# Optimization experiments

Measured on AMD Instinct MI355X. Metric: run time of the kernel, lower is better.

Reference implementation:

```python
import jax, jax.numpy as jnp
import numpy as np
import math

B, T, C = 2, 2048, 2048
H, KV, HD = 16, 4, 128          # n_head, n_kv_head, head_dim
REP = H // KV
FFN = 5632                      # multiple_of-rounded 2/3 * 4 * n_embd
EPS = 1e-5


def setup_inputs() -> dict:
    key = jax.random.key(0)
    ks = jax.random.split(key, 10)
    s = 0.02
    x = jax.random.normal(ks[0], (B, T, C), dtype=jnp.float32)
    # RoPE table: (T, HD/2, 2) = (cos, sin)
    inv_freq = 1.0 / (10000.0 ** (np.arange(0, HD, 2, dtype=np.float32) / HD))
    ang = np.arange(T, dtype=np.float32)[:, None] * inv_freq[None, :]
    freqs_cis = jnp.asarray(np.stack([np.cos(ang), np.sin(ang)], axis=-1))
    wq = s * jax.random.normal(ks[1], (H * HD, C), dtype=jnp.float32)
    wk = s * jax.random.normal(ks[2], (KV * HD, C), dtype=jnp.float32)
    wv = s * jax.random.normal(ks[3], (KV * HD, C), dtype=jnp.float32)
    wo = s * jax.random.normal(ks[4], (C, H * HD), dtype=jnp.float32)
    w1 = s * jax.random.normal(ks[5], (FFN, C), dtype=jnp.float32)
    w2 = s * jax.random.normal(ks[6], (FFN, C), dtype=jnp.float32)
    c_proj = s * jax.random.normal(ks[7], (C, FFN), dtype=jnp.float32)
    g1 = jnp.ones((C,), dtype=jnp.float32)
    g2 = jnp.ones((C,), dtype=jnp.float32)
    return {"x": x, "freqs_cis": freqs_cis, "wq": wq, "wk": wk, "wv": wv,
            "wo": wo, "w1": w1, "w2": w2, "c_proj": c_proj, "g1": g1, "g2": g2}


def _rmsnorm(x, g, eps=EPS):
    return x * jax.lax.rsqrt(jnp.mean(x * x, axis=-1, keepdims=True) + eps) * g


def _rope(t, freqs_cis):
    # t: (B, T, nH, HD); freqs_cis: (T, HD/2, 2)
    tr = t.reshape(*t.shape[:-1], HD // 2, 2)
    cos = freqs_cis[None, :, None, :, 0]
    sin = freqs_cis[None, :, None, :, 1]
    out = jnp.stack([tr[..., 0] * cos - tr[..., 1] * sin,
                     tr[..., 0] * sin + tr[..., 1] * cos], axis=-1)
    return out.reshape(t.shape)


def reference(x, freqs_cis, wq, wk, wv, wo, w1, w2, c_proj, g1, g2):
    h = _rmsnorm(x, g1)
    q = (h @ wq.T).reshape(B, T, H, HD)
    k = (h @ wk.T).reshape(B, T, KV, HD)
    v = (h @ wv.T).reshape(B, T, KV, HD)
    q = _rope(q, freqs_cis)
    k = _rope(k, freqs_cis)
    # GQA: group query heads by kv head; never materialize expanded K/V
    q = q.transpose(0, 2, 1, 3).reshape(B, KV, REP, T, HD)  # b g r q d
    k = k.transpose(0, 2, 1, 3)                              # b g k d
    v = v.transpose(0, 2, 1, 3)                              # b g k d
    scale = 1.0 / math.sqrt(HD)
    scores = jnp.einsum('bgrqd,bgkd->bgrqk', q, k) * scale
    causal = jnp.tril(jnp.ones((T, T), dtype=bool))
    scores = jnp.where(causal, scores, jnp.float32(-1e30))
    attn = jax.nn.softmax(scores, axis=-1)
    y = jnp.einsum('bgrqk,bgkd->bgrqd', attn, v)
    y = y.reshape(B, H, T, HD).transpose(0, 2, 1, 3).reshape(B, T, C)
    x = x + y @ wo.T
    h2 = _rmsnorm(x, g2)
    mlp = (jax.nn.silu(h2 @ w1.T) * (h2 @ w2.T)) @ c_proj.T
    return x + mlp
```

## Files before the change

### kernel.cpp

```cpp
#include <hip/hip_runtime.h>
#include <hip/hip_bf16.h>
#include <math.h>

#define TT   2048
#define CC   2048
#define NB   2
#define NH   16
#define NKV  4
#define HDIM 128
#define NFFN 5632

typedef __attribute__((ext_vector_type(8))) short     bf8;
typedef __attribute__((ext_vector_type(4))) float     f32x4;
typedef __attribute__((ext_vector_type(8))) unsigned short u16x8;
typedef __attribute__((ext_vector_type(4))) unsigned short u16x4;

__device__ __forceinline__ float b2f(unsigned short u) {
    union { unsigned u; float f; } v; v.u = ((unsigned)u) << 16; return v.f;
}
__device__ __forceinline__ unsigned short f2bf(float f) {
    union { float f; unsigned u; } v; v.f = f;
    unsigned r = (v.u + 0x7fffu + ((v.u >> 16) & 1u)) >> 16;
    return (unsigned short)r;
}
__device__ __forceinline__ void gll16(const void* g, void* l) {
    __builtin_amdgcn_global_load_lds((const __attribute__((address_space(1))) void*)g,
                                     (__attribute__((address_space(3))) void*)l, 16, 0, 0);
}

__global__ __launch_bounds__(256) void cvt_k(const float* __restrict__ in,
        __hip_bfloat16* __restrict__ out)
{
    const size_t i = ((size_t)blockIdx.x * 256 + threadIdx.x) * 8;
    float4 a = *(const float4*)(in + i);
    float4 b = *(const float4*)(in + i + 4);
    u16x8 v;
    v[0] = f2bf(a.x); v[1] = f2bf(a.y); v[2] = f2bf(a.z); v[3] = f2bf(a.w);
    v[4] = f2bf(b.x); v[5] = f2bf(b.y); v[6] = f2bf(b.z); v[7] = f2bf(b.w);
    *(u16x8*)((unsigned short*)out + i) = v;
}

__global__ __launch_bounds__(256) void cvt3_k(const float* __restrict__ wq,
        const float* __restrict__ wk, const float* __restrict__ wv,
        __hip_bfloat16* __restrict__ out)
{
    const int row = blockIdx.x;
    const float* src = (row < 2048) ? (wq + (size_t)row * CC)
                     : (row < 2560) ? (wk + (size_t)(row - 2048) * CC)
                                    : (wv + (size_t)(row - 2560) * CC);
    const int e0 = threadIdx.x * 8;
    float4 a = *(const float4*)(src + e0);
    float4 b = *(const float4*)(src + e0 + 4);
    u16x8 v;
    v[0] = f2bf(a.x); v[1] = f2bf(a.y); v[2] = f2bf(a.z); v[3] = f2bf(a.w);
    v[4] = f2bf(b.x); v[5] = f2bf(b.y); v[6] = f2bf(b.z); v[7] = f2bf(b.w);
    *(u16x8*)((unsigned short*)out + (size_t)row * CC + e0) = v;
}

__global__ __launch_bounds__(256) void rms_f32_k(const float* __restrict__ x,
        const float* __restrict__ g, __hip_bfloat16* __restrict__ o)
{
    const size_t row = blockIdx.x;
    const int e0 = threadIdx.x * 8;
    float4 a = *(const float4*)(x + row * CC + e0);
    float4 b = *(const float4*)(x + row * CC + e0 + 4);
    float vals[8] = {a.x, a.y, a.z, a.w, b.x, b.y, b.z, b.w};
    float s = 0.f;
    #pragma unroll
    for (int e = 0; e < 8; ++e) s += vals[e] * vals[e];
    #pragma unroll
    for (int off = 32; off; off >>= 1) s += __shfl_xor(s, off);
    __shared__ float wsum[4];
    if ((threadIdx.x & 63) == 0) wsum[threadIdx.x >> 6] = s;
    __syncthreads();
    float scale = rsqrtf((wsum[0] + wsum[1] + wsum[2] + wsum[3]) * (1.0f / CC) + 1e-5f);
    float4 g0 = *(const float4*)(g + e0);
    float4 g1 = *(const float4*)(g + e0 + 4);
    float gs[8] = {g0.x, g0.y, g0.z, g0.w, g1.x, g1.y, g1.z, g1.w};
    u16x8 ov;
    #pragma unroll
    for (int e = 0; e < 8; ++e) ov[e] = f2bf(vals[e] * scale * gs[e]);
    *(u16x8*)((unsigned short*)o + row * CC + e0) = ov;
}

__global__ __launch_bounds__(256) void rms_bf16_k(const __hip_bfloat16* __restrict__ x,
        const float* __restrict__ g, __hip_bfloat16* __restrict__ o)
{
    const size_t row = blockIdx.x;
    const int e0 = threadIdx.x * 8;
    u16x8 xv = *(const u16x8*)((const unsigned short*)x + row * CC + e0);
    float vals[8];
    #pragma unroll
    for (int e = 0; e < 8; ++e) vals[e] = b2f(xv[e]);
    float s = 0.f;
    #pragma unroll
    for (int e = 0; e < 8; ++e) s += vals[e] * vals[e];
    #pragma unroll
    for (int off = 32; off; off >>= 1) s += __shfl_xor(s, off);
    __shared__ float wsum[4];
    if ((threadIdx.x & 63) == 0) wsum[threadIdx.x >> 6] = s;
    __syncthreads();
    float scale = rsqrtf((wsum[0] + wsum[1] + wsum[2] + wsum[3]) * (1.0f / CC) + 1e-5f);
    float4 g0 = *(const float4*)(g + e0);
    float4 g1 = *(const float4*)(g + e0 + 4);
    float gs[8] = {g0.x, g0.y, g0.z, g0.w, g1.x, g1.y, g1.z, g1.w};
    u16x8 ov;
    #pragma unroll
    for (int e = 0; e < 8; ++e) ov[e] = f2bf(vals[e] * scale * gs[e]);
    *(u16x8*)((unsigned short*)o + row * CC + e0) = ov;
}

#define GBM 128
#define GBN 128
#define GBK 32

template<int EPI, int OUTB>
__global__ __launch_bounds__(256) void gemm_db(
        const __hip_bfloat16* __restrict__ A,
        const __hip_bfloat16* __restrict__ W,
        const void* __restrict__ Rp,
        void* __restrict__ Cp,
        int M, int N, int K)
{
    __shared__ alignas(16) __hip_bfloat16 As[2][GBM][GBK];
    __shared__ alignas(16) __hip_bfloat16 Ws[2][GBN][GBK];
    const int tid  = threadIdx.x;
    const int lane = tid & 63;
    const int wid  = tid >> 6;
    const int wr = wid >> 1, wc = wid & 1;
    const int nwg = gridDim.x * gridDim.y;
    const int lin = blockIdx.y * gridDim.x + blockIdx.x;
    const int nlin = (lin & 7) * (nwg >> 3) + (lin >> 3);
    const int bxs = nlin % gridDim.x, bys = nlin / gridDim.x;
    const int bm = bys * GBM, bn = bxs * GBN;
    const int l4  = lane >> 2;
    const int lk8 = (lane & 3) * 8;
    const int fr  = lane & 15;
    const int fk  = (lane >> 4) * 8;

    f32x4 acc[4][4];
    #pragma unroll
    for (int m = 0; m < 4; ++m)
        #pragma unroll
        for (int n = 0; n < 4; ++n) acc[m][n] = (f32x4){0.f, 0.f, 0.f, 0.f};

    const __hip_bfloat16* ga0 = A + (size_t)(bm + wid * 32 + l4) * K + lk8;
    const __hip_bfloat16* ga1 = A + (size_t)(bm + wid * 32 + 16 + l4) * K + lk8;
    const __hip_bfloat16* gw0 = W + (size_t)(bn + wid * 32 + l4) * K + lk8;
    const __hip_bfloat16* gw1 = W + (size_t)(bn + wid * 32 + 16 + l4) * K + lk8;

    const int nt = K >> 5;
    gll16(ga0, &As[0][wid * 32][0]);
    gll16(ga1, &As[0][wid * 32 + 16][0]);
    gll16(gw0, &Ws[0][wid * 32][0]);
    gll16(gw1, &Ws[0][wid * 32 + 16][0]);

    #pragma unroll 2
    for (int t = 0; t < nt; ++t) {
        const int cur = t & 1;
        __syncthreads();
        if (t + 1 < nt) {
            const int k1 = (t + 1) << 5;
            const int nx = cur ^ 1;
            gll16(ga0 + k1, &As[nx][wid * 32][0]);
            gll16(ga1 + k1, &As[nx][wid * 32 + 16][0]);
            gll16(gw0 + k1, &Ws[nx][wid * 32][0]);
            gll16(gw1 + k1, &Ws[nx][wid * 32 + 16][0]);
        }
        bf8 af[4];
        #pragma unroll
        for (int m = 0; m < 4; ++m)
            af[m] = *(const bf8*)&As[cur][wr * 64 + m * 16 + fr][fk];
        #pragma unroll
        for (int n = 0; n < 4; ++n) {
            bf8 wf = *(const bf8*)&Ws[cur][wc * 64 + n * 16 + fr][fk];
            #pragma unroll
            for (int m = 0; m < 4; ++m)
                acc[m][n] = __builtin_amdgcn_mfma_f32_16x16x32_bf16(af[m], wf, acc[m][n], 0, 0, 0);
        }
    }

    const int rj = (lane >> 4) * 4;
    #pragma unroll
    for (int m = 0; m < 4; ++m) {
        #pragma unroll
        for (int j = 0; j < 4; ++j) {
            const size_t row = (size_t)(bm + wr * 64 + m * 16 + rj + j);
            #pragma unroll
            for (int n = 0; n < 4; ++n) {
                const size_t col = (size_t)(bn + wc * 64 + n * 16 + fr);
                float v = acc[m][n][j];
                if (EPI == 1) v += ((const float*)Rp)[row * N + col];
                if (EPI == 2) v += b2f(((const unsigned short*)Rp)[row * N + col]);
                if (EPI == 3) {
                    float gv = b2f(((const unsigned short*)Rp)[row * N + col]);
                    v = (gv / (1.0f + __expf(-gv))) * v;
                }
                if (OUTB) ((unsigned short*)Cp)[row * N + col] = f2bf(v);
                else      ((float*)Cp)[row * N + col] = v;
            }
        }
    }
}

__global__ __launch_bounds__(256) void gemm_qkv_db(
        const __hip_bfloat16* __restrict__ A,
        const __hip_bfloat16* __restrict__ W,
        const float* __restrict__ fc,
        __hip_bfloat16* __restrict__ qo,
        __hip_bfloat16* __restrict__ ko,
        __hip_bfloat16* __restrict__ vto,
        int M, int K)
{
    __shared__ alignas(16) __hip_bfloat16 As[2][GBM][GBK];
    __shared__ alignas(16) __hip_bfloat16 Ws[2][GBN][GBK];
    const int tid  = threadIdx.x;
    const int lane = tid & 63;
    const int wid  = tid >> 6;
    const int wr = wid >> 1, wc = wid & 1;
    const int nwg = gridDim.x * gridDim.y;
    const int lin = blockIdx.y * gridDim.x + blockIdx.x;
    const int nlin = (lin & 7) * (nwg >> 3) + (lin >> 3);
    const int bxs = nlin % gridDim.x, bys = nlin / gridDim.x;
    const int bm = bys * GBM, bn = bxs * GBN;
    const int l4  = lane >> 2;
    const int lk8 = (lane & 3) * 8;
    const int fr  = lane & 15;
    const int fk  = (lane >> 4) * 8;

    f32x4 acc[4][4];
    #pragma unroll
    for (int m = 0; m < 4; ++m)
        #pragma unroll
        for (int n = 0; n < 4; ++n) acc[m][n] = (f32x4){0.f, 0.f, 0.f, 0.f};

    const __hip_bfloat16* ga0 = A + (size_t)(bm + wid * 32 + l4) * K + lk8;
    const __hip_bfloat16* ga1 = A + (size_t)(bm + wid * 32 + 16 + l4) * K + lk8;
    const __hip_bfloat16* gw0 = W + (size_t)(bn + wid * 32 + l4) * K + lk8;
    const __hip_bfloat16* gw1 = W + (size_t)(bn + wid * 32 + 16 + l4) * K + lk8;

    const int nt = K >> 5;
    gll16(ga0, &As[0][wid * 32][0]);
    gll16(ga1, &As[0][wid * 32 + 16][0]);
    gll16(gw0, &Ws[0][wid * 32][0]);
    gll16(gw1, &Ws[0][wid * 32 + 16][0]);

    #pragma unroll 2
    for (int t = 0; t < nt; ++t) {
        const int cur = t & 1;
        __syncthreads();
        if (t + 1 < nt) {
            const int k1 = (t + 1) << 5;
            const int nx = cur ^ 1;
            gll16(ga0 + k1, &As[nx][wid * 32][0]);
            gll16(ga1 + k1, &As[nx][wid * 32 + 16][0]);
            gll16(gw0 + k1, &Ws[nx][wid * 32][0]);
            gll16(gw1 + k1, &Ws[nx][wid * 32 + 16][0]);
        }
        bf8 af[4];
        #pragma unroll
        for (int m = 0; m < 4; ++m)
            af[m] = *(const bf8*)&As[cur][wr * 64 + m * 16 + fr][fk];
        #pragma unroll
        for (int n = 0; n < 4; ++n) {
            bf8 wf = *(const bf8*)&Ws[cur][wc * 64 + n * 16 + fr][fk];
            #pragma unroll
            for (int m = 0; m < 4; ++m)
                acc[m][n] = __builtin_amdgcn_mfma_f32_16x16x32_bf16(af[m], wf, acc[m][n], 0, 0, 0);
        }
    }

    const int rj = (lane >> 4) * 4;
    #pragma unroll
    for (int m = 0; m < 4; ++m) {
        #pragma unroll
        for (int n = 0; n < 4; ++n) {
            const int col = bn + wc * 64 + n * 16 + fr;
            const int row0 = bm + wr * 64 + m * 16 + rj;
            if (col < 2560) {
                const int i2 = ((col & 127) >> 1) * 2;
                const int role = col & 1;
                #pragma unroll
                for (int j = 0; j < 4; ++j) {
                    const int t0 = (row0 + j) & (TT - 1);
                    const float cv = fc[t0 * HDIM + i2];
                    const float sv = fc[t0 * HDIM + i2 + 1];
                    const float v = acc[m][n][j];
                    const float partner = __shfl_xor(v, 1);
                    const float o = role ? (partner * sv + v * cv) : (v * cv - partner * sv);
                    if (col < 2048)
                        ((unsigned short*)qo)[(size_t)(row0 + j) * CC + col] = f2bf(o);
                    else
                        ((unsigned short*)ko)[(size_t)(row0 + j) * (NKV * HDIM) + (col - 2048)] = f2bf(o);
                }
            } else {
                const int vc = col - 2560;
                const int g = vc >> 7, d = vc & 127;
                const int b = row0 >> 11, t0 = row0 & (TT - 1);
                unsigned short* vp = (unsigned short*)vto +
                    ((size_t)(b * NKV + g) * HDIM + d) * TT + t0;
                u16x4 ov;
                #pragma unroll
                for (int j = 0; j < 4; ++j) ov[j] = f2bf(acc[m][n][j]);
                *(u16x4*)vp = ov;
            }
        }
    }
}

#define PBM 128
#define PBN 256
#define PBK 64

template<int EPI, int OUTB>
__global__ __launch_bounds__(512) void gemm_8p(
        const __hip_bfloat16* __restrict__ A,
        const __hip_bfloat16* __restrict__ W,
        const void* __restrict__ Rp,
        void* __restrict__ Cp,
        int M, int N, int K)
{
    __shared__ alignas(16) __hip_bfloat16 As[2][PBM][PBK];
    __shared__ alignas(16) __hip_bfloat16 Ws[2][PBN][PBK];
    const int tid  = threadIdx.x;
    const int lane = tid & 63;
    const int wid  = tid >> 6;
    const int wr = wid >> 2, wc = wid & 3;
    const int nwg = gridDim.x * gridDim.y;
    const int lin = blockIdx.y * gridDim.x + blockIdx.x;
    const int nlin = (lin & 7) * (nwg >> 3) + (lin >> 3);
    const int bxs = nlin % gridDim.x, bys = nlin / gridDim.x;
    const int bm = bys * PBM, bn = bxs * PBN;
    const int fr = lane & 15;
    const int hi = lane >> 4;

    f32x4 acc[4][4];
    #pragma unroll
    for (int m = 0; m < 4; ++m)
        #pragma unroll
        for (int n = 0; n < 4; ++n) acc[m][n] = (f32x4){0.f, 0.f, 0.f, 0.f};

    const unsigned short* Ag = (const unsigned short*)A;
    const unsigned short* Wg = (const unsigned short*)W;

    auto STAGE = [&](int buf, int k0) {
        #pragma unroll
        for (int l = 0; l < 2; ++l) {
            const int s = l * 512 + tid;
            const int row = s >> 3;
            const int srcb = ((s & 7) * 16) ^ ((row & 7) << 4);
            gll16(Ag + (size_t)(bm + row) * K + k0 + (srcb >> 1),
                  (unsigned short*)&As[buf][0][0] + (l * 512 + wid * 64) * 8);
        }
        #pragma unroll
        for (int l = 0; l < 4; ++l) {
            const int s = l * 512 + tid;
            const int row = s >> 3;
            const int srcb = ((s & 7) * 16) ^ ((row & 7) << 4);
            gll16(Wg + (size_t)(bn + row) * K + k0 + (srcb >> 1),
                  (unsigned short*)&Ws[buf][0][0] + (l * 512 + wid * 64) * 8);
        }
    };

    const int nt = K >> 6;
    STAGE(0, 0);
    __syncthreads();

    for (int t = 0; t < nt; ++t) {
        const int cur = t & 1;
        const char* Ab = (const char*)&As[cur][0][0];
        const char* Bb = (const char*)&Ws[cur][0][0];

        bf8 bF[4][2];
        #pragma unroll
        for (int n = 0; n < 4; ++n) {
            const int row = wc * 64 + n * 16 + fr;
            #pragma unroll
            for (int kk = 0; kk < 2; ++kk) {
                const int off = (kk * 64 + hi * 16) ^ ((row & 7) << 4);
                bF[n][kk] = *(const bf8*)(Bb + row * 128 + off);
            }
        }
        bf8 a0, a1;
        {
            const int row = wr * 64 + fr;
            a0 = *(const bf8*)(Ab + row * 128 + ((hi * 16)      ^ ((row & 7) << 4)));
            a1 = *(const bf8*)(Ab + row * 128 + ((64 + hi * 16) ^ ((row & 7) << 4)));
        }
        if (t + 1 < nt) STAGE(cur ^ 1, (t + 1) * PBK);
        __builtin_amdgcn_s_barrier();
        __builtin_amdgcn_s_setprio(1);
        #pragma unroll
        for (int n = 0; n < 4; ++n) {
            acc[0][n] = __builtin_amdgcn_mfma_f32_16x16x32_bf16(a0, bF[n][0], acc[0][n], 0, 0, 0);
            acc[0][n] = __builtin_amdgcn_mfma_f32_16x16x32_bf16(a1, bF[n][1], acc[0][n], 0, 0, 0);
        }
        __builtin_amdgcn_s_setprio(0);
        __builtin_amdgcn_s_barrier();

        #pragma unroll
        for (int m = 1; m < 4; ++m) {
            const int row = wr * 64 + m * 16 + fr;
            bf8 am0 = *(const bf8*)(Ab + row * 128 + ((hi * 16)      ^ ((row & 7) << 4)));
            bf8 am1 = *(const bf8*)(Ab + row * 128 + ((64 + hi * 16) ^ ((row & 7) << 4)));
            __builtin_amdgcn_s_barrier();
            __builtin_amdgcn_s_setprio(1);
            #pragma unroll
            for (int n = 0; n < 4; ++n) {
                acc[m][n] = __builtin_amdgcn_mfma_f32_16x16x32_bf16(am0, bF[n][0], acc[m][n], 0, 0, 0);
                acc[m][n] = __builtin_amdgcn_mfma_f32_16x16x32_bf16(am1, bF[n][1], acc[m][n], 0, 0, 0);
            }
            __builtin_amdgcn_s_setprio(0);
            if (m < 3) __builtin_amdgcn_s_barrier();
        }
        __syncthreads();
    }

    const int rj = hi * 4;
    #pragma unroll
    for (int m = 0; m < 4; ++m) {
        #pragma unroll
        for (int j = 0; j < 4; ++j) {
            const size_t row = (size_t)(bm + wr * 64 + m * 16 + rj + j);
            #pragma unroll
            for (int n = 0; n < 4; ++n) {
                const size_t col = (size_t)(bn + wc * 64 + n * 16 + fr);
                float v = acc[m][n][j];
                if (EPI == 1) v += ((const float*)Rp)[row * N + col];
                if (EPI == 2) v += b2f(((const unsigned short*)Rp)[row * N + col]);
                if (EPI == 3) {
                    float gv = b2f(((const unsigned short*)Rp)[row * N + col]);
                    v = (gv / (1.0f + __expf(-gv))) * v;
                }
                if (OUTB) ((unsigned short*)Cp)[row * N + col] = f2bf(v);
                else      ((float*)Cp)[row * N + col] = v;
            }
        }
    }
}

#define AQB 128
#define AKV 64

__global__ __launch_bounds__(512) void attn_mfma(const __hip_bfloat16* __restrict__ q,
        const __hip_bfloat16* __restrict__ k, const __hip_bfloat16* __restrict__ vt,
        __hip_bfloat16* __restrict__ y)
{
    __shared__ alignas(16) unsigned short Ks[AKV * HDIM];
    __shared__ alignas(16) unsigned short Vs[HDIM * AKV];
    __shared__ alignas(16) unsigned short Ps[AQB * AKV];

    const int qt = (TT / AQB - 1) - blockIdx.x;
    const int h  = blockIdx.y;
    const int b  = blockIdx.z;
    const int g  = h >> 2;
    const int qbase = qt * AQB;

    const int tid  = threadIdx.x;
    const int lane = tid & 63;
    const int wid  = tid >> 6;
    const int fr   = lane & 15;
    const int fk8  = (lane >> 4) * 8;
    const int rj   = (lane >> 4) * 4;

    bf8 qf[4];
    {
        const unsigned short* qp = (const unsigned short*)q +
            (size_t)(b * TT + qbase + wid * 16 + fr) * CC + h * HDIM;
        #pragma unroll
        for (int c = 0; c < 4; ++c)
            qf[c] = *(const bf8*)(qp + c * 32 + fk8);
    }
    const unsigned short* vtb = (const unsigned short*)vt + (size_t)(b * NKV + g) * HDIM * TT;

    f32x4 oacc[8];
    float m_r[4], l_r[4];
    #pragma unroll
    for (int n = 0; n < 8; ++n) oacc[n] = (f32x4){0.f, 0.f, 0.f, 0.f};
    #pragma unroll
    for (int j = 0; j < 4; ++j) { m_r[j] = -1e30f; l_r[j] = 0.f; }

    const float scale = 0.08838834764831845f;
    const int ntiles = qbase / AKV + 2;
    const int kjr = tid >> 3;
    const int kkc = (tid & 7) * 16;
    const int vdr = tid >> 2;
    const int vjc = (tid & 3) * 16;

    u16x8 krg[2], vrg[2];
    auto LOADT = [&](int jb) {
        const unsigned short* kp = (const unsigned short*)k +
            ((size_t)(b * TT + jb + kjr) * (NKV * HDIM)) + g * HDIM + kkc;
        const unsigned short* vp = vtb + (size_t)vdr * TT + jb + vjc;
        #pragma unroll
        for (int c = 0; c < 2; ++c) {
            krg[c] = *(const u16x8*)(kp + c * 8);
            vrg[c] = *(const u16x8*)(vp + c * 8);
        }
    };
    auto WRITET = [&]() {
        #pragma unroll
        for (int c = 0; c < 2; ++c) {
            const int byteK = (kjr * 256 + (kkc + c * 8) * 2) ^ ((kjr & 7) << 4);
            *(u16x8*)((char*)Ks + byteK) = krg[c];
            const int byteV = (vdr * 128 + (vjc + c * 8) * 2) ^ ((vdr & 7) << 4);
            *(u16x8*)((char*)Vs + byteV) = vrg[c];
        }
    };

    LOADT(0);

    for (int tile = 0; tile < ntiles; ++tile) {
        __syncthreads();
        WRITET();
        if (tile + 1 < ntiles) LOADT((tile + 1) * AKV);
        __syncthreads();

        f32x4 s[4];
        #pragma unroll
        for (int n = 0; n < 4; ++n) s[n] = (f32x4){0.f, 0.f, 0.f, 0.f};
        __builtin_amdgcn_s_setprio(1);
        #pragma unroll
        for (int c = 0; c < 4; ++c) {
            #pragma unroll
            for (int n = 0; n < 4; ++n) {
                const int j = n * 16 + fr;
                const int byteB = (j * 256 + (c * 32 + fk8) * 2) ^ ((j & 7) << 4);
                bf8 kf = *(const bf8*)((char*)Ks + byteB);
                s[n] = __builtin_amdgcn_mfma_f32_16x16x32_bf16(qf[c], kf, s[n], 0, 0, 0);
            }
        }
        __builtin_amdgcn_s_setprio(0);

        const int jbase = tile * AKV;
        #pragma unroll
        for (int jj = 0; jj < 4; ++jj) {
            const int qg = qbase + wid * 16 + rj + jj;
            float sv[4];
            #pragma unroll
            for (int n = 0; n < 4; ++n) {
                const int jg = jbase + n * 16 + fr;
                sv[n] = (jg <= qg) ? s[n][jj] * scale : -1e30f;
            }
            float tmax = fmaxf(fmaxf(sv[0], sv[1]), fmaxf(sv[2], sv[3]));
            tmax = fmaxf(tmax, __shfl_xor(tmax, 1));
            tmax = fmaxf(tmax, __shfl_xor(tmax, 2));
            tmax = fmaxf(tmax, __shfl_xor(tmax, 4));
            tmax = fmaxf(tmax, __shfl_xor(tmax, 8));
            if (tmax > m_r[jj] + 8.0f) {
                const float alpha = __expf(m_r[jj] - tmax);
                m_r[jj] = tmax;
                l_r[jj] *= alpha;
                #pragma unroll
                for (int n = 0; n < 8; ++n) oacc[n][jj] *= alpha;
            }
            const float mnew = m_r[jj];
            const int prow = wid * 16 + rj + jj;
            float tsum = 0.f;
            #pragma unroll
            for (int n = 0; n < 4; ++n) {
                const float p = __expf(sv[n] - mnew);
                tsum += p;
                const int byteP = (prow * 128 + (n * 16 + fr) * 2) ^ ((prow & 7) << 4);
                *(unsigned short*)((char*)Ps + byteP) = f2bf(p);
            }
            tsum += __shfl_xor(tsum, 1);
            tsum += __shfl_xor(tsum, 2);
            tsum += __shfl_xor(tsum, 4);
            tsum += __shfl_xor(tsum, 8);
            l_r[jj] += tsum;
        }

        __builtin_amdgcn_s_setprio(1);
        #pragma unroll
        for (int c2 = 0; c2 < 2; ++c2) {
            const int prow = wid * 16 + fr;
            const int byteA = (prow * 128 + (c2 * 32 + fk8) * 2) ^ ((prow & 7) << 4);
            bf8 pf = *(const bf8*)((char*)Ps + byteA);
            #pragma unroll
            for (int n = 0; n < 8; ++n) {
                const int d = n * 16 + fr;
                const int byteB = (d * 128 + (c2 * 32 + fk8) * 2) ^ ((d & 7) << 4);
                bf8 vf = *(const bf8*)((char*)Vs + byteB);
                oacc[n] = __builtin_amdgcn_mfma_f32_16x16x32_bf16(pf, vf, oacc[n], 0, 0, 0);
            }
        }
        __builtin_amdgcn_s_setprio(0);
    }

    #pragma unroll
    for (int jj = 0; jj < 4; ++jj) {
        const float inv = 1.0f / l_r[jj];
        unsigned short* yrow = (unsigned short*)y +
            ((size_t)(b * TT + qbase + wid * 16 + rj + jj) * CC) + h * HDIM;
        #pragma unroll
        for (int n = 0; n < 8; ++n)
            yrow[n * 16 + fr] = f2bf(oacc[n][jj] * inv);
    }
}

extern "C" void kernel_launch(void* const* d_in, const int* in_sizes, int n_in,
                              void* d_out, int out_size, void* d_ws, size_t ws_size,
                              hipStream_t stream)
{
    (void)in_sizes; (void)n_in; (void)out_size; (void)ws_size;
    const float* x     = (const float*)d_in[0];
    const float* fc    = (const float*)d_in[1];
    const float* wq    = (const float*)d_in[2];
    const float* wk    = (const float*)d_in[3];
    const float* wv    = (const float*)d_in[4];
    const float* wo    = (const float*)d_in[5];
    const float* w1    = (const float*)d_in[6];
    const float* w2    = (const float*)d_in[7];
    const float* cproj = (const float*)d_in[8];
    const float* g1    = (const float*)d_in[9];
    const float* g2    = (const float*)d_in[10];
    float* out = (float*)d_out;

    const int ROWS = NB * TT;
    unsigned char* wsb = (unsigned char*)d_ws;
    __hip_bfloat16* x2b = (__hip_bfloat16*)(wsb);
    __hip_bfloat16* hb  = (__hip_bfloat16*)(wsb + 16777216u);
    __hip_bfloat16* w1b = (__hip_bfloat16*)(wsb + 33554432u);
    __hip_bfloat16* w2b = (__hip_bfloat16*)(wsb + 56623104u);
    __hip_bfloat16* G1  = (__hip_bfloat16*)(wsb + 79691776u);
    __hip_bfloat16* cpb = w1b;
    __hip_bfloat16* qb   = (__hip_bfloat16*)(wsb + 33554432u);
    __hip_bfloat16* kb   = (__hip_bfloat16*)(wsb + 50331648u);
    __hip_bfloat16* vtb  = (__hip_bfloat16*)(wsb + 54525952u);
    __hip_bfloat16* yb   = (__hip_bfloat16*)(wsb + 58720256u);
    __hip_bfloat16* wbuf = (__hip_bfloat16*)(wsb + 75497472u);

    rms_f32_k<<<ROWS, 256, 0, stream>>>(x, g1, hb);
    cvt3_k<<<3072, 256, 0, stream>>>(wq, wk, wv, wbuf);
    gemm_qkv_db<<<dim3(3072 / GBN, ROWS / GBM), 256, 0, stream>>>(hb, wbuf, fc, qb, kb, vtb, ROWS, CC);
    attn_mfma<<<dim3(TT / AQB, NH, NB), 512, 0, stream>>>(qb, kb, vtb, yb);
    cvt_k<<<(CC * CC) / 2048, 256, 0, stream>>>(wo, wbuf);
    gemm_8p<1, 1><<<dim3(CC / PBN, ROWS / PBM), 512, 0, stream>>>(yb, wbuf, x, x2b, ROWS, CC, CC);
    rms_bf16_k<<<ROWS, 256, 0, stream>>>(x2b, g2, hb);
    cvt_k<<<(NFFN * CC) / 2048, 256, 0, stream>>>(w1, w1b);
    cvt_k<<<(NFFN * CC) / 2048, 256, 0, stream>>>(w2, w2b);
    gemm_8p<0, 1><<<dim3(NFFN / PBN, ROWS / PBM), 512, 0, stream>>>(hb, w1b, nullptr, G1, ROWS, NFFN, CC);
    gemm_8p<3, 1><<<dim3(NFFN / PBN, ROWS / PBM), 512, 0, stream>>>(hb, w2b, G1, G1, ROWS, NFFN, CC);
    cvt_k<<<(CC * NFFN) / 2048, 256, 0, stream>>>(cproj, cpb);
    gemm_8p<2, 0><<<dim3(CC / PBN, ROWS / PBM), 512, 0, stream>>>(G1, cpb, x2b, out, ROWS, CC, NFFN);
}
```

Baseline: 662.8 us.

## Transpose attention score MFMA so each lane owns one query row; merge w1/w2 casts

Swaps the MFMA operands in the QK^T product so the score accumulator is transposed and each lane holds one query row across its keys. The row max and row sum then need two cross-lane shuffles instead of four per row, and the online-softmax state shrinks to one scalar per lane. The rescale factors are broadcast back with shuffles only when some lane triggers a rescale. It also fuses the two FFN weight bf16 conversion launches into one kernel to save a launch; the P writes to LDS now use a different access pattern, which may change bank conflicts.

```diff
diff --git a/kernel.cpp b/kernel.cpp
--- a/kernel.cpp
+++ b/kernel.cpp
@@ -55,6 +55,24 @@
     v[0] = f2bf(a.x); v[1] = f2bf(a.y); v[2] = f2bf(a.z); v[3] = f2bf(a.w);
     v[4] = f2bf(b.x); v[5] = f2bf(b.y); v[6] = f2bf(b.z); v[7] = f2bf(b.w);
     *(u16x8*)((unsigned short*)out + (size_t)row * CC + e0) = v;
+}
+
+__global__ __launch_bounds__(256) void cvt2_k(const float* __restrict__ w1,
+        const float* __restrict__ w2,
+        __hip_bfloat16* __restrict__ o1, __hip_bfloat16* __restrict__ o2)
+{
+    const int row = blockIdx.x;
+    const float* src;
+    unsigned short* dst;
+    if (row < NFFN) { src = w1 + (size_t)row * CC; dst = (unsigned short*)o1 + (size_t)row * CC; }
+    else            { src = w2 + (size_t)(row - NFFN) * CC; dst = (unsigned short*)o2 + (size_t)(row - NFFN) * CC; }
+    const int e0 = threadIdx.x * 8;
+    float4 a = *(const float4*)(src + e0);
+    float4 b = *(const float4*)(src + e0 + 4);
+    u16x8 v;
+    v[0] = f2bf(a.x); v[1] = f2bf(a.y); v[2] = f2bf(a.z); v[3] = f2bf(a.w);
+    v[4] = f2bf(b.x); v[5] = f2bf(b.y); v[6] = f2bf(b.z); v[7] = f2bf(b.w);
+    *(u16x8*)(dst + e0) = v;
 }
 
 __global__ __launch_bounds__(256) void rms_f32_k(const float* __restrict__ x,
@@ -474,11 +492,9 @@
     const unsigned short* vtb = (const unsigned short*)vt + (size_t)(b * NKV + g) * HDIM * TT;
 
     f32x4 oacc[8];
-    float m_r[4], l_r[4];
+    float m_r = -1e30f, l_r = 0.f;
     #pragma unroll
     for (int n = 0; n < 8; ++n) oacc[n] = (f32x4){0.f, 0.f, 0.f, 0.f};
-    #pragma unroll
-    for (int j = 0; j < 4; ++j) { m_r[j] = -1e30f; l_r[j] = 0.f; }
 
     const float scale = 0.08838834764831845f;
     const int ntiles = qbase / AKV + 2;
@@ -486,6 +502,8 @@
     const int kkc = (tid & 7) * 16;
     const int vdr = tid >> 2;
     const int vjc = (tid & 3) * 16;
+    const int qg = qbase + wid * 16 + fr;
+    const int prow = wid * 16 + fr;
 
     u16x8 krg[2], vrg[2];
     auto LOADT = [&](int jb) {
@@ -527,54 +545,54 @@
                 const int j = n * 16 + fr;
                 const int byteB = (j * 256 + (c * 32 + fk8) * 2) ^ ((j & 7) << 4);
                 bf8 kf = *(const bf8*)((char*)Ks + byteB);
-                s[n] = __builtin_amdgcn_mfma_f32_16x16x32_bf16(qf[c], kf, s[n], 0, 0, 0);
+                s[n] = __builtin_amdgcn_mfma_f32_16x16x32_bf16(kf, qf[c], s[n], 0, 0, 0);
             }
         }
         __builtin_amdgcn_s_setprio(0);
 
         const int jbase = tile * AKV;
-        #pragma unroll
-        for (int jj = 0; jj < 4; ++jj) {
-            const int qg = qbase + wid * 16 + rj + jj;
-            float sv[4];
-            #pragma unroll
-            for (int n = 0; n < 4; ++n) {
-                const int jg = jbase + n * 16 + fr;
-                sv[n] = (jg <= qg) ? s[n][jj] * scale : -1e30f;
-            }
-            float tmax = fmaxf(fmaxf(sv[0], sv[1]), fmaxf(sv[2], sv[3]));
-            tmax = fmaxf(tmax, __shfl_xor(tmax, 1));
-            tmax = fmaxf(tmax, __shfl_xor(tmax, 2));
-            tmax = fmaxf(tmax, __shfl_xor(tmax, 4));
-            tmax = fmaxf(tmax, __shfl_xor(tmax, 8));
-            if (tmax > m_r[jj] + 8.0f) {
-                const float alpha = __expf(m_r[jj] - tmax);
-                m_r[jj] = tmax;
-                l_r[jj] *= alpha;
+        float sv[4][4];
+        float tmax = -1e30f;
+        #pragma unroll
+        for (int n = 0; n < 4; ++n)
+            #pragma unroll
+            for (int j = 0; j < 4; ++j) {
+                const int jg = jbase + n * 16 + rj + j;
+                sv[n][j] = (jg <= qg) ? s[n][j] * scale : -1e30f;
+                tmax = fmaxf(tmax, sv[n][j]);
+            }
+        tmax = fmaxf(tmax, __shfl_xor(tmax, 16));
+        tmax = fmaxf(tmax, __shfl_xor(tmax, 32));
+        const bool trig = tmax > m_r + 8.0f;
+        if (__any(trig)) {
+            const float alpha = trig ? __expf(m_r - tmax) : 1.0f;
+            if (trig) m_r = tmax;
+            l_r *= alpha;
+            float aj[4];
+            #pragma unroll
+            for (int j = 0; j < 4; ++j) aj[j] = __shfl(alpha, rj + j);
+            #pragma unroll
+            for (int n = 0; n < 8; ++n)
                 #pragma unroll
-                for (int n = 0; n < 8; ++n) oacc[n][jj] *= alpha;
-            }
-            const float mnew = m_r[jj];
-            const int prow = wid * 16 + rj + jj;
-            float tsum = 0.f;
-            #pragma unroll
-            for (int n = 0; n < 4; ++n) {
-                const float p = __expf(sv[n] - mnew);
+                for (int j = 0; j < 4; ++j) oacc[n][j] *= aj[j];
+        }
+        float tsum = 0.f;
+        #pragma unroll
+        for (int n = 0; n < 4; ++n)
+            #pragma unroll
+            for (int j = 0; j < 4; ++j) {
+                const float p = __expf(sv[n][j] - m_r);
                 tsum += p;
-                const int byteP = (prow * 128 + (n * 16 + fr) * 2) ^ ((prow & 7) << 4);
+                const int byteP = (prow * 128 + (n * 16 + rj + j) * 2) ^ ((prow & 7) << 4);
                 *(unsigned short*)((char*)Ps + byteP) = f2bf(p);
             }
-            tsum += __shfl_xor(tsum, 1);
-            tsum += __shfl_xor(tsum, 2);
-            tsum += __shfl_xor(tsum, 4);
-            tsum += __shfl_xor(tsum, 8);
-            l_r[jj] += tsum;
-        }
+        tsum += __shfl_xor(tsum, 16);
+        tsum += __shfl_xor(tsum, 32);
+        l_r += tsum;
 
         __builtin_amdgcn_s_setprio(1);
         #pragma unroll
         for (int c2 = 0; c2 < 2; ++c2) {
-            const int prow = wid * 16 + fr;
             const int byteA = (prow * 128 + (c2 * 32 + fk8) * 2) ^ ((prow & 7) << 4);
             bf8 pf = *(const bf8*)((char*)Ps + byteA);
             #pragma unroll
@@ -588,9 +606,10 @@
         __builtin_amdgcn_s_setprio(0);
     }
 
+    const float rl = 1.0f / l_r;
     #pragma unroll
     for (int jj = 0; jj < 4; ++jj) {
-        const float inv = 1.0f / l_r[jj];
+        const float inv = __shfl(rl, rj + jj);
         unsigned short* yrow = (unsigned short*)y +
             ((size_t)(b * TT + qbase + wid * 16 + rj + jj) * CC) + h * HDIM;
         #pragma unroll
@@ -638,8 +657,7 @@
     cvt_k<<<(CC * CC) / 2048, 256, 0, stream>>>(wo, wbuf);
     gemm_8p<1, 1><<<dim3(CC / PBN, ROWS / PBM), 512, 0, stream>>>(yb, wbuf, x, x2b, ROWS, CC, CC);
     rms_bf16_k<<<ROWS, 256, 0, stream>>>(x2b, g2, hb);
-    cvt_k<<<(NFFN * CC) / 2048, 256, 0, stream>>>(w1, w1b);
-    cvt_k<<<(NFFN * CC) / 2048, 256, 0, stream>>>(w2, w2b);
+    cvt2_k<<<2 * NFFN, 256, 0, stream>>>(w1, w2, w1b, w2b);
     gemm_8p<0, 1><<<dim3(NFFN / PBN, ROWS / PBM), 512, 0, stream>>>(hb, w1b, nullptr, G1, ROWS, NFFN, CC);
     gemm_8p<3, 1><<<dim3(NFFN / PBN, ROWS / PBM), 512, 0, stream>>>(hb, w2b, G1, G1, ROWS, NFFN, CC);
     cvt_k<<<(CC * NFFN) / 2048, 256, 0, stream>>>(cproj, cpb);
```

Result: faster. 620.2 us (-6.4%).
